# Kernel optimization log

Measured on AMD Instinct MI355X. Metric: run time of the kernel, lower is better.

The kernel has to match this reference:

```python
import jax, jax.numpy as jnp
import numpy as np

B, C, INTER, T, H, W = 2, 256, 64, 8, 32, 32


def setup_inputs() -> dict:
    key = jax.random.key(0)
    ks = jax.random.split(key, 4)
    scale_q = 1.0 / np.sqrt(C)
    x = jax.random.normal(ks[0], (B, C, T, H, W), dtype=jnp.float32)
    Wq = jax.random.normal(ks[1], (INTER, C), dtype=jnp.float32) * scale_q
    Wk = jax.random.normal(ks[2], (INTER, C), dtype=jnp.float32) * scale_q
    Wv = jax.random.normal(ks[3], (C, C), dtype=jnp.float32) * scale_q
    return {
        "x": x,
        "Wq": Wq, "bq": jnp.zeros((INTER,), jnp.float32),
        "Wk": Wk, "bk": jnp.zeros((INTER,), jnp.float32),
        "Wv": Wv, "bv": jnp.zeros((C,), jnp.float32),
    }


def reference(x, Wq, bq, Wk, bk, Wv, bv):
    b, c, t, h, w = x.shape
    n = t * h * w
    xf = x.reshape(b, c, n)  # [B, C, N] (row-major flatten over T,H,W)
    # 1x1x1 Conv3d == per-voxel linear projection
    q = jnp.einsum('oc,bcn->bno', Wq, xf) + bq          # [B, N, INTER]
    k = jnp.einsum('oc,bcn->bon', Wk, xf) + bk[:, None]  # [B, INTER, N]
    v = jnp.einsum('oc,bcn->bon', Wv, xf) + bv[:, None]  # [B, C, N]
    energy = jnp.einsum('bid,bdj->bij', q, k)            # [B, N, N]
    attention = jax.nn.softmax(energy, axis=-1)
    # out[b,c,i] = sum_j v[b,c,j] * attention[b,i,j]
    out = jnp.einsum('bcj,bij->bci', v, attention)       # [B, C, N]
    out = out.reshape(b, c, t, h, w) + x
    return out
```

## Files before the change

kernel.cpp:

```cpp
#include <hip/hip_runtime.h>
#include <hip/hip_bf16.h>

typedef short short8 __attribute__((ext_vector_type(8)));
typedef float float4v __attribute__((ext_vector_type(4)));

#define MFMA(a, b, c) __builtin_amdgcn_mfma_f32_16x16x32_bf16((a), (b), (c), 0, 0, 0)

typedef const __attribute__((address_space(1))) unsigned int gu32;
typedef __attribute__((address_space(3))) unsigned int lu32;
#define GLOAD_LDS16(g, l) __builtin_amdgcn_global_load_lds((gu32*)(g), (lu32*)(l), 16, 0, 0)

#define VMWAIT(n) asm volatile("s_waitcnt vmcnt(" n ")" ::: "memory")

#define LOG2E 1.4426950408889634f

static __device__ __forceinline__ unsigned short f2bf(float f) {
    union { float f; unsigned u; } v; v.f = f;
    unsigned r = (v.u + 0x7fffu + ((v.u >> 16) & 1u)) >> 16;
    return (unsigned short)r;
}
static __device__ __forceinline__ float bf2f(unsigned short h) {
    union { unsigned u; float f; } v; v.u = ((unsigned)h) << 16;
    return v.f;
}
static __device__ __forceinline__ unsigned pk2bf(float a, float b) {
    union { __hip_bfloat162 h; unsigned u; } cv;
    cv.h = __float22bfloat162_rn(make_float2(a, b));
    return cv.u;
}

static __device__ __forceinline__ int qk_idx(int b, int n, int o) {
    int frag = (b * 512 + (n >> 4)) * 2 + (o >> 5);
    return frag * 512 + ((o >> 3) & 3) * 128 + (n & 15) * 8 + (o & 7);
}
static __device__ __forceinline__ int v_idx(int b, int c, int n) {
    int frag = (b * 256 + (n >> 5)) * 16 + (c >> 4);
    return frag * 512 + ((n >> 3) & 3) * 128 + (c & 15) * 8 + (n & 7);
}

__global__ void wcvt(const float* __restrict__ Wq, const float* __restrict__ Wk,
                     const float* __restrict__ Wv,
                     unsigned short* __restrict__ Whi, unsigned short* __restrict__ Wlo) {
    int idx = blockIdx.x * 256 + threadIdx.x;
    if (idx >= 384 * 256) return;
    int row = idx >> 8, c = idx & 255;
    float f;
    if (row < 64)       f = Wq[row * 256 + c];
    else if (row < 128) f = Wk[(row - 64) * 256 + c];
    else                f = Wv[(row - 128) * 256 + c];
    unsigned short hi = f2bf(f);
    Whi[idx] = hi;
    if (row < 128) Wlo[idx] = f2bf(f - bf2f(hi));
}

__global__ __launch_bounds__(256, 1) void proj(
        const float* __restrict__ x, const unsigned short* __restrict__ Whi,
        const unsigned short* __restrict__ Wlo,
        const float* __restrict__ bq, const float* __restrict__ bk,
        const float* __restrict__ bv,
        unsigned short* __restrict__ qhi_ws, unsigned short* __restrict__ qlo_ws,
        unsigned short* __restrict__ khi_ws, unsigned short* __restrict__ klo_ws,
        unsigned short* __restrict__ vws) {
    __shared__ unsigned short XThi[64 * 264];
    __shared__ unsigned short XTlo[64 * 264];

    const int tid = threadIdx.x;
    const int b  = blockIdx.x >> 7;
    const int n0 = (blockIdx.x & 127) << 6;
    const float* xb = x + b * 2097152;

    for (int p = 0; p < 16; ++p) {
        int idx = p * 256 + tid;
        int c = idx >> 4, nq = idx & 15;
        float4v xv = *reinterpret_cast<const float4v*>(xb + c * 8192 + n0 + nq * 4);
#pragma unroll
        for (int q = 0; q < 4; ++q) {
            unsigned short hi = f2bf(xv[q]);
            XThi[(nq * 4 + q) * 264 + c] = hi;
            XTlo[(nq * 4 + q) * 264 + c] = f2bf(xv[q] - bf2f(hi));
        }
    }
    __syncthreads();

    const int lane = tid & 63, w = tid >> 6;
    const int quad = lane >> 4, l16 = lane & 15;

    short8 aXhi[8], aXlo[8];
#pragma unroll
    for (int ks = 0; ks < 8; ++ks) {
        aXhi[ks] = *reinterpret_cast<const short8*>(&XThi[(w * 16 + l16) * 264 + ks * 32 + quad * 8]);
        aXlo[ks] = *reinterpret_cast<const short8*>(&XTlo[(w * 16 + l16) * 264 + ks * 32 + quad * 8]);
    }

#pragma unroll
    for (int ot = 0; ot < 8; ++ot) {
        float4v acc = {0.f, 0.f, 0.f, 0.f};
#pragma unroll
        for (int ks = 0; ks < 8; ++ks) {
            short8 bwhi = *reinterpret_cast<const short8*>(&Whi[(ot * 16 + l16) * 256 + ks * 32 + quad * 8]);
            short8 bwlo = *reinterpret_cast<const short8*>(&Wlo[(ot * 16 + l16) * 256 + ks * 32 + quad * 8]);
            acc = MFMA(aXhi[ks], bwhi, acc);
            acc = MFMA(aXlo[ks], bwhi, acc);
            acc = MFMA(aXhi[ks], bwlo, acc);
        }
        int o = ot * 16 + l16;
        float bias = (ot < 4) ? bq[o] : bk[o - 64];
#pragma unroll
        for (int r = 0; r < 4; ++r) {
            int n = n0 + w * 16 + quad * 4 + r;
            float y = acc[r] + bias;
            if (ot < 4) y *= LOG2E;
            unsigned short hi = f2bf(y);
            unsigned short lo = f2bf(y - bf2f(hi));
            if (ot < 4) {
                int id = qk_idx(b, n, o);
                qhi_ws[id] = hi; qlo_ws[id] = lo;
            } else {
                int id = qk_idx(b, n, o - 64);
                khi_ws[id] = hi; klo_ws[id] = lo;
            }
        }
    }

    float4v acc2[4][4];
#pragma unroll
    for (int mt = 0; mt < 4; ++mt)
#pragma unroll
        for (int nt = 0; nt < 4; ++nt) acc2[mt][nt] = (float4v){0.f, 0.f, 0.f, 0.f};

#pragma unroll
    for (int ks = 0; ks < 8; ++ks) {
        short8 aW[4], bX[4];
#pragma unroll
        for (int mt = 0; mt < 4; ++mt)
            aW[mt] = *reinterpret_cast<const short8*>(&Whi[(128 + w * 64 + mt * 16 + l16) * 256 + ks * 32 + quad * 8]);
#pragma unroll
        for (int nt = 0; nt < 4; ++nt)
            bX[nt] = *reinterpret_cast<const short8*>(&XThi[(nt * 16 + l16) * 264 + ks * 32 + quad * 8]);
#pragma unroll
        for (int mt = 0; mt < 4; ++mt)
#pragma unroll
            for (int nt = 0; nt < 4; ++nt)
                acc2[mt][nt] = MFMA(aW[mt], bX[nt], acc2[mt][nt]);
    }
#pragma unroll
    for (int mt = 0; mt < 4; ++mt) {
#pragma unroll
        for (int r = 0; r < 4; ++r) {
            int c = w * 64 + mt * 16 + quad * 4 + r;
            float bias = bv[c];
#pragma unroll
            for (int nt = 0; nt < 4; ++nt) {
                int n = n0 + nt * 16 + l16;
                vws[v_idx(b, c, n)] = f2bf(acc2[mt][nt][r] + bias);
            }
        }
    }
}

__global__ __launch_bounds__(256, 2) void attn(
        const unsigned short* __restrict__ qhi_ws, const unsigned short* __restrict__ qlo_ws,
        const unsigned short* __restrict__ khi_ws, const unsigned short* __restrict__ klo_ws,
        const unsigned short* __restrict__ vws,
        unsigned short* __restrict__ Opart, float* __restrict__ ml) {
    __shared__ unsigned short Vlds[3][8192];
    __shared__ unsigned short Klds[3][4096];
    __shared__ unsigned short Pl[4 * 32 * 32];

    const int tid = threadIdx.x, lane = tid & 63, w = tid >> 6;
    const int quad = lane >> 4, l16 = lane & 15;
    const int xcd = blockIdx.x & 7, b = xcd & 1, jr = xcd >> 1;
    const int it = blockIdx.x >> 3;
    const int iw16 = it * 8 + w * 2;
    unsigned short* Pw = Pl + w * (32 * 32);

    const unsigned short* qhb = qhi_ws + (size_t)((b * 512 + iw16) * 2) * 512 + lane * 8;
    const unsigned short* qlb = qlo_ws + (size_t)((b * 512 + iw16) * 2) * 512 + lane * 8;
    short8 qh[2][2], ql[2][2];
#pragma unroll
    for (int mt = 0; mt < 2; ++mt)
#pragma unroll
        for (int kf = 0; kf < 2; ++kf) {
            qh[mt][kf] = *reinterpret_cast<const short8*>(qhb + (mt * 2 + kf) * 512);
            ql[mt][kf] = *reinterpret_cast<const short8*>(qlb + (mt * 2 + kf) * 512);
        }

    const unsigned short* khs = khi_ws + (size_t)((b * 512 + jr * 128) * 2) * 512 + w * 512 + lane * 8;
    const unsigned short* kls = klo_ws + (size_t)((b * 512 + jr * 128) * 2) * 512 + w * 512 + lane * 8;
    const unsigned short* vstage = vws + ((size_t)(b * 256 + jr * 64) * 16 + w * 4) * 512 + lane * 8;

    float4v acc[2][16];
#pragma unroll
    for (int mt = 0; mt < 2; ++mt)
#pragma unroll
        for (int cf = 0; cf < 16; ++cf) acc[mt][cf] = (float4v){0.f, 0.f, 0.f, 0.f};
    float lrow[2][4];
    short8 aP[2];
#pragma unroll
    for (int mt = 0; mt < 2; ++mt)
#pragma unroll
        for (int r = 0; r < 4; ++r) lrow[mt][r] = 0.f;

    GLOAD_LDS16(khs, &Klds[0][w * 512]);
    GLOAD_LDS16(kls, &Klds[0][2048 + w * 512]);
#pragma unroll
    for (int q = 0; q < 4; ++q)
        GLOAD_LDS16(vstage + q * 512, &Vlds[0][(w * 4 + q) * 512]);
    GLOAD_LDS16(khs + 2048, &Klds[1][w * 512]);
    GLOAD_LDS16(kls + 2048, &Klds[1][2048 + w * 512]);
    khs += 4096; kls += 4096; vstage += 8192;

    int bprev = 2, bcur = 0, bnext = 1;
    int kc = 0, kst = 2;
#pragma unroll 1
    for (int itn = 0; itn < 64; ++itn) {
        if (itn < 63) VMWAIT("6");
        else          VMWAIT("4");
        __builtin_amdgcn_s_barrier();
        __builtin_amdgcn_sched_barrier(0);

        if (itn < 63) {
#pragma unroll
            for (int q = 0; q < 4; ++q)
                GLOAD_LDS16(vstage + q * 512, &Vlds[bnext][(w * 4 + q) * 512]);
            vstage += 8192;
        }
        if (itn < 62) {
            GLOAD_LDS16(khs, &Klds[kst][w * 512]);
            GLOAD_LDS16(kls, &Klds[kst][2048 + w * 512]);
            khs += 2048; kls += 2048;
        }

        const unsigned short* Kc = &Klds[kc][0];
        float4v s[2][2];
#pragma unroll
        for (int mt = 0; mt < 2; ++mt)
#pragma unroll
            for (int jt = 0; jt < 2; ++jt) s[mt][jt] = (float4v){0.f, 0.f, 0.f, 0.f};
        __builtin_amdgcn_s_setprio(1);
#pragma unroll
        for (int jt = 0; jt < 2; ++jt) {
            short8 kh0 = *reinterpret_cast<const short8*>(Kc + (jt * 2 + 0) * 512 + lane * 8);
            short8 kh1 = *reinterpret_cast<const short8*>(Kc + (jt * 2 + 1) * 512 + lane * 8);
            short8 kl0 = *reinterpret_cast<const short8*>(Kc + 2048 + (jt * 2 + 0) * 512 + lane * 8);
            short8 kl1 = *reinterpret_cast<const short8*>(Kc + 2048 + (jt * 2 + 1) * 512 + lane * 8);
#pragma unroll
            for (int mt = 0; mt < 2; ++mt) {
                s[mt][jt] = MFMA(qh[mt][0], kh0, s[mt][jt]);
                s[mt][jt] = MFMA(ql[mt][0], kh0, s[mt][jt]);
                s[mt][jt] = MFMA(qh[mt][0], kl0, s[mt][jt]);
                s[mt][jt] = MFMA(qh[mt][1], kh1, s[mt][jt]);
                s[mt][jt] = MFMA(ql[mt][1], kh1, s[mt][jt]);
                s[mt][jt] = MFMA(qh[mt][1], kl1, s[mt][jt]);
            }
        }
        __builtin_amdgcn_s_setprio(0);

        if (itn) {
            const unsigned short* vl = &Vlds[bprev][0];
            __builtin_amdgcn_s_setprio(1);
#pragma unroll
            for (int cf = 0; cf < 16; ++cf) {
                short8 v0 = *reinterpret_cast<const short8*>(vl + cf * 512 + lane * 8);
                acc[0][cf] = MFMA(aP[0], v0, acc[0][cf]);
                acc[1][cf] = MFMA(aP[1], v0, acc[1][cf]);
            }
            __builtin_amdgcn_s_setprio(0);
        }

#pragma unroll
        for (int mt = 0; mt < 2; ++mt)
#pragma unroll
            for (int jt = 0; jt < 2; ++jt) {
                float p0 = exp2f(s[mt][jt][0]);
                float p1 = exp2f(s[mt][jt][1]);
                float p2 = exp2f(s[mt][jt][2]);
                float p3 = exp2f(s[mt][jt][3]);
                lrow[mt][0] += p0; lrow[mt][1] += p1;
                lrow[mt][2] += p2; lrow[mt][3] += p3;
                unsigned u01 = pk2bf(p0, p1);
                unsigned u23 = pk2bf(p2, p3);
                int base = (mt * 16 + quad * 4) * 32 + jt * 16 + l16;
                Pw[base]       = (unsigned short)u01;
                Pw[base + 32]  = (unsigned short)(u01 >> 16);
                Pw[base + 64]  = (unsigned short)u23;
                Pw[base + 96]  = (unsigned short)(u23 >> 16);
            }

#pragma unroll
        for (int mt = 0; mt < 2; ++mt)
            aP[mt] = *reinterpret_cast<const short8*>(&Pw[(mt * 16 + l16) * 32 + quad * 8]);

        int t = bprev; bprev = bcur; bcur = bnext; bnext = t;
        kc  = (kc  == 2) ? 0 : kc + 1;
        kst = (kst == 2) ? 0 : kst + 1;
    }

    VMWAIT("0");
    __builtin_amdgcn_s_barrier();
    __builtin_amdgcn_sched_barrier(0);
    {
        const unsigned short* vl = &Vlds[bprev][0];
#pragma unroll
        for (int cf = 0; cf < 16; ++cf) {
            short8 v0 = *reinterpret_cast<const short8*>(vl + cf * 512 + lane * 8);
            acc[0][cf] = MFMA(aP[0], v0, acc[0][cf]);
            acc[1][cf] = MFMA(aP[1], v0, acc[1][cf]);
        }
    }

#pragma unroll
    for (int mt = 0; mt < 2; ++mt)
#pragma unroll
        for (int r = 0; r < 4; ++r) {
            float lv = lrow[mt][r];
            lv += __shfl_xor(lv, 1);
            lv += __shfl_xor(lv, 2);
            lv += __shfl_xor(lv, 4);
            lv += __shfl_xor(lv, 8);
            if (l16 == 0) {
                int iloc = w * 32 + mt * 16 + quad * 4 + r;
                ml[blockIdx.x * 128 + iloc] = lv;
            }
        }

    unsigned short* ob = Opart + (size_t)blockIdx.x * 32768;
#pragma unroll
    for (int mt = 0; mt < 2; ++mt)
#pragma unroll
        for (int cf = 0; cf < 16; ++cf) {
            unsigned u01 = pk2bf(acc[mt][cf][0], acc[mt][cf][1]);
            unsigned u23 = pk2bf(acc[mt][cf][2], acc[mt][cf][3]);
            int iloc = w * 32 + mt * 16 + quad * 4;
            ob[(iloc + 0) * 256 + cf * 16 + l16] = (unsigned short)u01;
            ob[(iloc + 1) * 256 + cf * 16 + l16] = (unsigned short)(u01 >> 16);
            ob[(iloc + 2) * 256 + cf * 16 + l16] = (unsigned short)u23;
            ob[(iloc + 3) * 256 + cf * 16 + l16] = (unsigned short)(u23 >> 16);
        }
}

__global__ __launch_bounds__(256) void combine(
        const unsigned short* __restrict__ Opart, const float* __restrict__ ml,
        const float* __restrict__ x, float* __restrict__ out) {
    __shared__ float fac[128];
    __shared__ float trans[64 * 130];

    const int t = threadIdx.x;
    const int blk = blockIdx.x;
    const int b = blk & 1, cc = (blk >> 1) & 3, it = blk >> 3;

    if (t < 128) {
        float sum = 0.f;
#pragma unroll
        for (int s = 0; s < 4; ++s)
            sum += ml[(size_t)((it << 3) | (s << 1) | b) * 128 + t];
        fac[t] = 1.0f / sum;
    }
    __syncthreads();

    {
        const int cgrp = t & 7, irow = t >> 3;
#pragma unroll
        for (int ip = 0; ip < 4; ++ip) {
            int i = ip * 32 + irow;
            float a[8];
#pragma unroll
            for (int e = 0; e < 8; ++e) a[e] = 0.f;
#pragma unroll
            for (int s = 0; s < 4; ++s) {
                const unsigned short* op = Opart +
                    (size_t)((it << 3) | (s << 1) | b) * 32768 + i * 256 + cc * 64 + cgrp * 8;
                short8 o = *reinterpret_cast<const short8*>(op);
#pragma unroll
                for (int e = 0; e < 8; ++e) a[e] += bf2f((unsigned short)o[e]);
            }
            float f = fac[i];
#pragma unroll
            for (int e = 0; e < 8; ++e) trans[(cgrp * 8 + e) * 130 + i] = a[e] * f;
        }
    }
    __syncthreads();

    {
        const int c2 = t >> 2, iq = t & 3;
        const int cg = cc * 64 + c2;
        const float* xr = x + (size_t)b * 2097152 + (size_t)cg * 8192 + it * 128;
        float* orow = out + (size_t)b * 2097152 + (size_t)cg * 8192 + it * 128;
#pragma unroll 2
        for (int k = 0; k < 8; ++k) {
            int i = iq * 4 + k * 16;
            float4v o;
#pragma unroll
            for (int r = 0; r < 4; ++r) o[r] = trans[c2 * 130 + i + r];
            float4v xv = *reinterpret_cast<const float4v*>(xr + i);
#pragma unroll
            for (int r = 0; r < 4; ++r) o[r] += xv[r];
            *reinterpret_cast<float4v*>(orow + i) = o;
        }
    }
}

extern "C" void kernel_launch(void* const* d_in, const int* in_sizes, int n_in,
                              void* d_out, int out_size, void* d_ws, size_t ws_size,
                              hipStream_t stream) {
    const float* x  = (const float*)d_in[0];
    const float* Wq = (const float*)d_in[1];
    const float* bq = (const float*)d_in[2];
    const float* Wk = (const float*)d_in[3];
    const float* bk = (const float*)d_in[4];
    const float* Wv = (const float*)d_in[5];
    const float* bv = (const float*)d_in[6];

    unsigned short* Whi = (unsigned short*)d_ws;
    unsigned short* Wlo = Whi + 384 * 256;
    unsigned short* qhi = Wlo + 128 * 256;
    unsigned short* qlo = qhi + 2 * 8192 * 64;
    unsigned short* khi = qlo + 2 * 8192 * 64;
    unsigned short* klo = khi + 2 * 8192 * 64;
    unsigned short* vws = klo + 2 * 8192 * 64;
    unsigned short* Opart = vws + 2 * 256 * 8192;
    float* ml = (float*)(Opart + (size_t)512 * 32768);

    wcvt<<<384, 256, 0, stream>>>(Wq, Wk, Wv, Whi, Wlo);
    proj<<<256, 256, 0, stream>>>(x, Whi, Wlo, bq, bk, bv, qhi, qlo, khi, klo, vws);
    attn<<<512, 256, 0, stream>>>(qhi, qlo, khi, klo, vws, Opart, ml);
    combine<<<512, 256, 0, stream>>>(Opart, ml, x, (float*)d_out);
}
```

Before: 234.2 us.

## Compute transposed QK^T so P feeds PV MFMA directly from registers

Swaps the MFMA operand order for the score computation so each lane holds scores along the key dimension, and permutes the K workspace layout so the resulting register layout matches the A-operand layout of the P·V MFMA. This removes the per-iteration LDS round trip for P (scalar stores plus reloads) and the LDS buffer, and simplifies the row-sum reduction to two cross-quad shuffles. The exchange is a producer-side index permutation for K, plus reliance on the permuted key order matching the V order exactly.

```diff
diff --git a/kernel.cpp b/kernel.cpp
--- a/kernel.cpp
+++ b/kernel.cpp
@@ -116,7 +116,9 @@
                 int id = qk_idx(b, n, o);
                 qhi_ws[id] = hi; qlo_ws[id] = lo;
             } else {
-                int id = qk_idx(b, n, o - 64);
+                int j = n & 31;
+                int nper = (n & ~31) | ((j & 4) << 2) | ((j >> 3) << 2) | (j & 3);
+                int id = qk_idx(b, nper, o - 64);
                 khi_ws[id] = hi; klo_ws[id] = lo;
             }
         }
@@ -165,14 +167,12 @@
         unsigned short* __restrict__ Opart, float* __restrict__ ml) {
     __shared__ unsigned short Vlds[3][8192];
     __shared__ unsigned short Klds[3][4096];
-    __shared__ unsigned short Pl[4 * 32 * 32];
 
     const int tid = threadIdx.x, lane = tid & 63, w = tid >> 6;
     const int quad = lane >> 4, l16 = lane & 15;
     const int xcd = blockIdx.x & 7, b = xcd & 1, jr = xcd >> 1;
     const int it = blockIdx.x >> 3;
     const int iw16 = it * 8 + w * 2;
-    unsigned short* Pw = Pl + w * (32 * 32);
 
     const unsigned short* qhb = qhi_ws + (size_t)((b * 512 + iw16) * 2) * 512 + lane * 8;
     const unsigned short* qlb = qlo_ws + (size_t)((b * 512 + iw16) * 2) * 512 + lane * 8;
@@ -194,12 +194,8 @@
     for (int mt = 0; mt < 2; ++mt)
 #pragma unroll
         for (int cf = 0; cf < 16; ++cf) acc[mt][cf] = (float4v){0.f, 0.f, 0.f, 0.f};
-    float lrow[2][4];
+    float lrow[2] = {0.f, 0.f};
     short8 aP[2];
-#pragma unroll
-    for (int mt = 0; mt < 2; ++mt)
-#pragma unroll
-        for (int r = 0; r < 4; ++r) lrow[mt][r] = 0.f;
 
     GLOAD_LDS16(khs, &Klds[0][w * 512]);
     GLOAD_LDS16(kls, &Klds[0][2048 + w * 512]);
@@ -246,12 +242,12 @@
             short8 kl1 = *reinterpret_cast<const short8*>(Kc + 2048 + (jt * 2 + 1) * 512 + lane * 8);
 #pragma unroll
             for (int mt = 0; mt < 2; ++mt) {
-                s[mt][jt] = MFMA(qh[mt][0], kh0, s[mt][jt]);
-                s[mt][jt] = MFMA(ql[mt][0], kh0, s[mt][jt]);
-                s[mt][jt] = MFMA(qh[mt][0], kl0, s[mt][jt]);
-                s[mt][jt] = MFMA(qh[mt][1], kh1, s[mt][jt]);
-                s[mt][jt] = MFMA(ql[mt][1], kh1, s[mt][jt]);
-                s[mt][jt] = MFMA(qh[mt][1], kl1, s[mt][jt]);
+                s[mt][jt] = MFMA(kh0, qh[mt][0], s[mt][jt]);
+                s[mt][jt] = MFMA(kh0, ql[mt][0], s[mt][jt]);
+                s[mt][jt] = MFMA(kl0, qh[mt][0], s[mt][jt]);
+                s[mt][jt] = MFMA(kh1, qh[mt][1], s[mt][jt]);
+                s[mt][jt] = MFMA(kh1, ql[mt][1], s[mt][jt]);
+                s[mt][jt] = MFMA(kl1, qh[mt][1], s[mt][jt]);
             }
         }
         __builtin_amdgcn_s_setprio(0);
@@ -269,27 +265,23 @@
         }
 
 #pragma unroll
-        for (int mt = 0; mt < 2; ++mt)
-#pragma unroll
-            for (int jt = 0; jt < 2; ++jt) {
-                float p0 = exp2f(s[mt][jt][0]);
-                float p1 = exp2f(s[mt][jt][1]);
-                float p2 = exp2f(s[mt][jt][2]);
-                float p3 = exp2f(s[mt][jt][3]);
-                lrow[mt][0] += p0; lrow[mt][1] += p1;
-                lrow[mt][2] += p2; lrow[mt][3] += p3;
-                unsigned u01 = pk2bf(p0, p1);
-                unsigned u23 = pk2bf(p2, p3);
-                int base = (mt * 16 + quad * 4) * 32 + jt * 16 + l16;
-                Pw[base]       = (unsigned short)u01;
-                Pw[base + 32]  = (unsigned short)(u01 >> 16);
-                Pw[base + 64]  = (unsigned short)u23;
-                Pw[base + 96]  = (unsigned short)(u23 >> 16);
-            }
-
-#pragma unroll
-        for (int mt = 0; mt < 2; ++mt)
-            aP[mt] = *reinterpret_cast<const short8*>(&Pw[(mt * 16 + l16) * 32 + quad * 8]);
+        for (int mt = 0; mt < 2; ++mt) {
+            float p0 = exp2f(s[mt][0][0]);
+            float p1 = exp2f(s[mt][0][1]);
+            float p2 = exp2f(s[mt][0][2]);
+            float p3 = exp2f(s[mt][0][3]);
+            float p4 = exp2f(s[mt][1][0]);
+            float p5 = exp2f(s[mt][1][1]);
+            float p6 = exp2f(s[mt][1][2]);
+            float p7 = exp2f(s[mt][1][3]);
+            lrow[mt] += (p0 + p1) + (p2 + p3) + (p4 + p5) + (p6 + p7);
+            union { short8 s8; unsigned u[4]; } ap;
+            ap.u[0] = pk2bf(p0, p1);
+            ap.u[1] = pk2bf(p2, p3);
+            ap.u[2] = pk2bf(p4, p5);
+            ap.u[3] = pk2bf(p6, p7);
+            aP[mt] = ap.s8;
+        }
 
         int t = bprev; bprev = bcur; bcur = bnext; bnext = t;
         kc  = (kc  == 2) ? 0 : kc + 1;
@@ -310,19 +302,13 @@
     }
 
 #pragma unroll
-    for (int mt = 0; mt < 2; ++mt)
-#pragma unroll
-        for (int r = 0; r < 4; ++r) {
-            float lv = lrow[mt][r];
-            lv += __shfl_xor(lv, 1);
-            lv += __shfl_xor(lv, 2);
-            lv += __shfl_xor(lv, 4);
-            lv += __shfl_xor(lv, 8);
-            if (l16 == 0) {
-                int iloc = w * 32 + mt * 16 + quad * 4 + r;
-                ml[blockIdx.x * 128 + iloc] = lv;
-            }
-        }
+    for (int mt = 0; mt < 2; ++mt) {
+        float lv = lrow[mt];
+        lv += __shfl_xor(lv, 16);
+        lv += __shfl_xor(lv, 32);
+        if (quad == 0)
+            ml[blockIdx.x * 128 + w * 32 + mt * 16 + l16] = lv;
+    }
 
     unsigned short* ob = Opart + (size_t)blockIdx.x * 32768;
 #pragma unroll
```

New measurement: 227.0 us, median of 2. -3.1%, faster.
